# Performance work log

Measured on AMD Instinct MI355X. Metric: run time of the kernel, lower is better.

The kernel has to match this reference:

```python
import jax, jax.numpy as jnp
import numpy as np

N_WIRES = 4
N_LAYERS = 3
N_PATCH = 196  # 14x14 2x2 patches of a 28x28 image


def setup_inputs() -> dict:
    key = jax.random.key(0)
    k1, k2, k3 = jax.random.split(key, 3)
    B = 8192
    x = jax.random.uniform(k1, (B, 28, 28), dtype=jnp.float32)
    theta = jax.random.normal(k2, (N_LAYERS, N_WIRES), dtype=jnp.float32) * 0.1
    W = jax.random.normal(k3, (10, 4 * 14 * 14), dtype=jnp.float32) * 0.02
    b = jnp.zeros((10,), jnp.float32)
    return {"x": x, "theta": theta, "W": W, "b": b}


def _apply_ry(state, theta, wire):
    # state: (B, P, 2, 2, 2, 2); RY(theta) = [[cos t/2, -sin t/2], [sin t/2, cos t/2]]
    ax = 2 + wire
    half = theta * 0.5
    c, s = jnp.cos(half), jnp.sin(half)
    if jnp.ndim(c):  # per-(B,P) encoder angle: broadcast over the 3 remaining wire axes
        c = c[..., None, None, None]
        s = s[..., None, None, None]
    s0 = jax.lax.index_in_dim(state, 0, ax, keepdims=False)
    s1 = jax.lax.index_in_dim(state, 1, ax, keepdims=False)
    return jnp.stack([c * s0 - s * s1, s * s0 + c * s1], axis=ax)


def _quanv(x, theta):
    B = x.shape[0]
    # 2x2 stride-2 patches, row-major over (r, c); within-patch order
    # [x[r,c], x[r,c+1], x[r+1,c], x[r+1,c+1]]
    patches = x.reshape(B, 14, 2, 14, 2).transpose(0, 1, 3, 2, 4).reshape(B, N_PATCH, 4)
    # encoder resets to |0000>; all gates are real RY, so amplitudes stay real
    state = jnp.zeros((B, N_PATCH, 2, 2, 2, 2), x.dtype).at[:, :, 0, 0, 0, 0].set(1.0)
    for w in range(N_WIRES):  # encoder: RY(data_w) on wire w
        state = _apply_ry(state, patches[:, :, w], w)
    for l in range(N_LAYERS):  # variational layers: RY(theta[l,w]) on wire w
        for w in range(N_WIRES):
            state = _apply_ry(state, theta[l, w], w)
    probs = state * state  # (B, P, 2,2,2,2), real amplitudes
    meas = []
    for w in range(N_WIRES):  # <Z_w> = P(wire w = 0) - P(wire w = 1)
        other = tuple(a for a in range(2, 6) if a != 2 + w)
        p = probs.sum(axis=other)  # (B, P, 2)
        meas.append(p[..., 0] - p[..., 1])
    return jnp.stack(meas, axis=-1).reshape(B, N_PATCH * N_WIRES)  # (B, 784)


def reference(x, theta, W, b):
    feats = _quanv(x, theta)            # (B, 784)
    logits = feats @ W.T + b            # (B, 10)
    return jax.nn.log_softmax(logits, axis=-1)
```

## Files before the change

kernel.cpp:

```cpp
#include <hip/hip_runtime.h>
#include <math.h>

#define NPIX 784
#define NCLS 10
#define ROWS 8
#define LPR 32
#define BLOCK 256

__global__ __launch_bounds__(256)
void quanv_fused_kernel(const float* __restrict__ x,
                        const float* __restrict__ theta,
                        const float* __restrict__ W,
                        const float* __restrict__ bias,
                        float* __restrict__ out) {
    __shared__ float Wl[NCLS * NPIX];
    __shared__ float Tl[NPIX];
    int tid = threadIdx.x;

    for (int idx4 = tid; idx4 < (NCLS * NPIX) / 4; idx4 += BLOCK) {
        float4 wv = reinterpret_cast<const float4*>(W)[idx4];
        int idx = idx4 << 2;
        int k = idx / NPIX;
        int p = idx - k * NPIX;
        int patch = p >> 2;
        int pr = patch / 14, pc = patch - pr * 14;
        int q0 = (pr * 28 + pc) * 2;
        float* dst = &Wl[k * NPIX + q0];
        dst[0]  = wv.x;  dst[1]  = wv.y;
        dst[28] = wv.z;  dst[29] = wv.w;
    }
    float t0 = theta[0] + theta[4] + theta[8];
    float t1 = theta[1] + theta[5] + theta[9];
    float t2 = theta[2] + theta[6] + theta[10];
    float t3 = theta[3] + theta[7] + theta[11];
    for (int q = tid; q < NPIX; q += BLOCK) {
        int i = q / 28;
        int j = q - i * 28;
        float ta = (i & 1) ? t2 : t0;
        float tb = (i & 1) ? t3 : t1;
        Tl[q] = (j & 1) ? tb : ta;
    }
    __syncthreads();

    int tx = tid & (LPR - 1);
    int row = blockIdx.x * ROWS + (tid >> 5);
    const float* xr = x + (size_t)row * NPIX;

    float acc[NCLS];
#pragma unroll
    for (int k = 0; k < NCLS; ++k) acc[k] = 0.f;

#pragma unroll
    for (int s = 0; s < 6; ++s) {
        int p = (tx + (s << 5)) << 2;
        float4 xv = *reinterpret_cast<const float4*>(xr + p);
        float4 tv = *reinterpret_cast<const float4*>(&Tl[p]);
        float f0 = __cosf(xv.x + tv.x);
        float f1 = __cosf(xv.y + tv.y);
        float f2 = __cosf(xv.z + tv.z);
        float f3 = __cosf(xv.w + tv.w);
#pragma unroll
        for (int k = 0; k < NCLS; ++k) {
            float4 wv = *reinterpret_cast<const float4*>(&Wl[k * NPIX + p]);
            acc[k] += f0 * wv.x + f1 * wv.y + f2 * wv.z + f3 * wv.w;
        }
    }
    if (tx < 4) {
        int p = (tx + 192) << 2;
        float4 xv = *reinterpret_cast<const float4*>(xr + p);
        float4 tv = *reinterpret_cast<const float4*>(&Tl[p]);
        float f0 = __cosf(xv.x + tv.x);
        float f1 = __cosf(xv.y + tv.y);
        float f2 = __cosf(xv.z + tv.z);
        float f3 = __cosf(xv.w + tv.w);
#pragma unroll
        for (int k = 0; k < NCLS; ++k) {
            float4 wv = *reinterpret_cast<const float4*>(&Wl[k * NPIX + p]);
            acc[k] += f0 * wv.x + f1 * wv.y + f2 * wv.z + f3 * wv.w;
        }
    }

#pragma unroll
    for (int k = 0; k < NCLS; ++k) {
        float v = acc[k];
        v += __shfl_xor(v, 1);
        v += __shfl_xor(v, 2);
        v += __shfl_xor(v, 4);
        v += __shfl_xor(v, 8);
        v += __shfl_xor(v, 16);
        acc[k] = v;
    }

    if (tx == 0) {
        float logits[NCLS];
        float m = -1e30f;
#pragma unroll
        for (int k = 0; k < NCLS; ++k) {
            logits[k] = acc[k] + bias[k];
            m = fmaxf(m, logits[k]);
        }
        float sum = 0.f;
#pragma unroll
        for (int k = 0; k < NCLS; ++k) sum += expf(logits[k] - m);
        float lse = m + logf(sum);
#pragma unroll
        for (int k = 0; k < NCLS; ++k) out[row * NCLS + k] = logits[k] - lse;
    }
}

extern "C" void kernel_launch(void* const* d_in, const int* in_sizes, int n_in,
                              void* d_out, int out_size, void* d_ws, size_t ws_size,
                              hipStream_t stream) {
    const float* x     = (const float*)d_in[0];
    const float* theta = (const float*)d_in[1];
    const float* W     = (const float*)d_in[2];
    const float* bias  = (const float*)d_in[3];
    float* out = (float*)d_out;

    int B = in_sizes[0] / NPIX;
    int grid = B / ROWS;
    quanv_fused_kernel<<<grid, BLOCK, 0, stream>>>(x, theta, W, bias, out);
}
```

Before: 80.88 us.

## Process two rows per warp and store W in original patch order

Each 32-lane group now handles two batch rows, so every W float4 read from shared memory is reused for two rows. W is copied into shared memory in its original patch-major order, and x is gathered per patch with float2 loads, which removes the scatter remap and the theta table. The summed theta angles stay in registers. In exchange, x loads shrink from float4 to strided float2, register pressure rises from the doubled accumulators, and the grid is half as large.

```diff
diff --git a/kernel.cpp b/kernel.cpp
--- a/kernel.cpp
+++ b/kernel.cpp
@@ -3,8 +3,7 @@
 
 #define NPIX 784
 #define NCLS 10
-#define ROWS 8
-#define LPR 32
+#define ROWS 16
 #define BLOCK 256
 
 __global__ __launch_bounds__(256)
@@ -14,89 +13,73 @@
                         const float* __restrict__ bias,
                         float* __restrict__ out) {
     __shared__ float Wl[NCLS * NPIX];
-    __shared__ float Tl[NPIX];
     int tid = threadIdx.x;
 
-    for (int idx4 = tid; idx4 < (NCLS * NPIX) / 4; idx4 += BLOCK) {
-        float4 wv = reinterpret_cast<const float4*>(W)[idx4];
-        int idx = idx4 << 2;
-        int k = idx / NPIX;
-        int p = idx - k * NPIX;
-        int patch = p >> 2;
-        int pr = patch / 14, pc = patch - pr * 14;
-        int q0 = (pr * 28 + pc) * 2;
-        float* dst = &Wl[k * NPIX + q0];
-        dst[0]  = wv.x;  dst[1]  = wv.y;
-        dst[28] = wv.z;  dst[29] = wv.w;
-    }
+    const float4* W4 = reinterpret_cast<const float4*>(W);
+    float4* Wl4 = reinterpret_cast<float4*>(Wl);
+    for (int i = tid; i < (NCLS * NPIX) / 4; i += BLOCK) Wl4[i] = W4[i];
+
     float t0 = theta[0] + theta[4] + theta[8];
     float t1 = theta[1] + theta[5] + theta[9];
     float t2 = theta[2] + theta[6] + theta[10];
     float t3 = theta[3] + theta[7] + theta[11];
-    for (int q = tid; q < NPIX; q += BLOCK) {
-        int i = q / 28;
-        int j = q - i * 28;
-        float ta = (i & 1) ? t2 : t0;
-        float tb = (i & 1) ? t3 : t1;
-        Tl[q] = (j & 1) ? tb : ta;
-    }
     __syncthreads();
 
-    int tx = tid & (LPR - 1);
-    int row = blockIdx.x * ROWS + (tid >> 5);
-    const float* xr = x + (size_t)row * NPIX;
+    int tx = tid & 31;
+    int g  = tid >> 5;
+    int row0 = blockIdx.x * ROWS + g * 2;
+    const float* xr0 = x + (size_t)row0 * NPIX;
+    const float* xr1 = xr0 + NPIX;
 
-    float acc[NCLS];
+    float acc0[NCLS], acc1[NCLS];
 #pragma unroll
-    for (int k = 0; k < NCLS; ++k) acc[k] = 0.f;
+    for (int k = 0; k < NCLS; ++k) { acc0[k] = 0.f; acc1[k] = 0.f; }
 
 #pragma unroll
-    for (int s = 0; s < 6; ++s) {
-        int p = (tx + (s << 5)) << 2;
-        float4 xv = *reinterpret_cast<const float4*>(xr + p);
-        float4 tv = *reinterpret_cast<const float4*>(&Tl[p]);
-        float f0 = __cosf(xv.x + tv.x);
-        float f1 = __cosf(xv.y + tv.y);
-        float f2 = __cosf(xv.z + tv.z);
-        float f3 = __cosf(xv.w + tv.w);
+    for (int s = 0; s < 7; ++s) {
+        int p = tx + (s << 5);
+        bool active = (s < 6) | (tx < 4);
+        if (active) {
+            int pr = p / 14;
+            int pc = p - pr * 14;
+            int off0 = pr * 56 + pc * 2;
+            int off1 = off0 + 28;
+            float2 a0 = *reinterpret_cast<const float2*>(xr0 + off0);
+            float2 b0 = *reinterpret_cast<const float2*>(xr0 + off1);
+            float2 a1 = *reinterpret_cast<const float2*>(xr1 + off0);
+            float2 b1 = *reinterpret_cast<const float2*>(xr1 + off1);
+            float f00 = __cosf(a0.x + t0), f01 = __cosf(a0.y + t1);
+            float f02 = __cosf(b0.x + t2), f03 = __cosf(b0.y + t3);
+            float f10 = __cosf(a1.x + t0), f11 = __cosf(a1.y + t1);
+            float f12 = __cosf(b1.x + t2), f13 = __cosf(b1.y + t3);
 #pragma unroll
-        for (int k = 0; k < NCLS; ++k) {
-            float4 wv = *reinterpret_cast<const float4*>(&Wl[k * NPIX + p]);
-            acc[k] += f0 * wv.x + f1 * wv.y + f2 * wv.z + f3 * wv.w;
-        }
-    }
-    if (tx < 4) {
-        int p = (tx + 192) << 2;
-        float4 xv = *reinterpret_cast<const float4*>(xr + p);
-        float4 tv = *reinterpret_cast<const float4*>(&Tl[p]);
-        float f0 = __cosf(xv.x + tv.x);
-        float f1 = __cosf(xv.y + tv.y);
-        float f2 = __cosf(xv.z + tv.z);
-        float f3 = __cosf(xv.w + tv.w);
-#pragma unroll
-        for (int k = 0; k < NCLS; ++k) {
-            float4 wv = *reinterpret_cast<const float4*>(&Wl[k * NPIX + p]);
-            acc[k] += f0 * wv.x + f1 * wv.y + f2 * wv.z + f3 * wv.w;
+            for (int k = 0; k < NCLS; ++k) {
+                float4 wv = *reinterpret_cast<const float4*>(&Wl[k * NPIX + (p << 2)]);
+                acc0[k] += f00 * wv.x + f01 * wv.y + f02 * wv.z + f03 * wv.w;
+                acc1[k] += f10 * wv.x + f11 * wv.y + f12 * wv.z + f13 * wv.w;
+            }
         }
     }
 
 #pragma unroll
     for (int k = 0; k < NCLS; ++k) {
-        float v = acc[k];
-        v += __shfl_xor(v, 1);
-        v += __shfl_xor(v, 2);
-        v += __shfl_xor(v, 4);
-        v += __shfl_xor(v, 8);
-        v += __shfl_xor(v, 16);
-        acc[k] = v;
+        float v0 = acc0[k], v1 = acc1[k];
+        v0 += __shfl_xor(v0, 1);  v1 += __shfl_xor(v1, 1);
+        v0 += __shfl_xor(v0, 2);  v1 += __shfl_xor(v1, 2);
+        v0 += __shfl_xor(v0, 4);  v1 += __shfl_xor(v1, 4);
+        v0 += __shfl_xor(v0, 8);  v1 += __shfl_xor(v1, 8);
+        v0 += __shfl_xor(v0, 16); v1 += __shfl_xor(v1, 16);
+        acc0[k] = v0; acc1[k] = v1;
     }
 
-    if (tx == 0) {
+    if (tx == 0 || tx == 16) {
+        const float* a = (tx == 0) ? acc0 : acc1;
+        int row = (tx == 0) ? row0 : row0 + 1;
         float logits[NCLS];
         float m = -1e30f;
 #pragma unroll
         for (int k = 0; k < NCLS; ++k) {
-            logits[k] = acc[k] + bias[k];
+            logits[k] = a[k] + bias[k];
             m = fmaxf(m, logits[k]);
         }
         float sum = 0.f;
```

Result: no change. 79.49 us, median of 2 (-1.7%).
